# Kernel optimization log

Measured on AMD Instinct MI355X. Metric: run time of the kernel, lower is better.

Reference implementation:

```python
import jax, jax.numpy as jnp
import numpy as np
from jax import lax

B = 8192
NQ = 4  # num_qubits
TWO_PI = 2.0 * np.pi
BN_EPS = 1e-5
ANG_EPS = 1e-6


def setup_inputs() -> dict:
    key = jax.random.key(0)
    ks = jax.random.split(key, 8)
    rn = lambda k, shape, s: jax.random.normal(k, shape, jnp.float32) * s
    return {
        "x": jax.random.normal(ks[0], (B, 1, 28, 28), jnp.float32),
        "conv1_w": rn(ks[1], (8, 1, 3, 3), 0.3),
        "conv1_b": jnp.zeros((8,), jnp.float32),
        "conv2_w": rn(ks[2], (16, 8, 3, 3), 0.1),
        "conv2_b": jnp.zeros((16,), jnp.float32),
        "fc1_w": rn(ks[3], (64, 16 * 7 * 7), 0.04),
        "fc1_b": jnp.zeros((64,), jnp.float32),
        "fc2_w": rn(ks[4], (NQ, 64), 0.12),
        "fc2_b": jnp.zeros((NQ,), jnp.float32),
        "bn_gamma": jnp.ones((NQ,), jnp.float32),
        "bn_beta": jnp.zeros((NQ,), jnp.float32),
        "var_params": jax.random.uniform(ks[5], (3 * NQ,), jnp.float32, 0.0, TWO_PI),
    }


# ---- batched 4-qubit statevector simulation (replaces per-sample Aer loop) ----

def _rx(t):
    c, s = jnp.cos(t / 2), jnp.sin(t / 2)
    return jnp.stack([jnp.stack([c + 0j, -1j * s], -1),
                      jnp.stack([-1j * s, c + 0j], -1)], -2).astype(jnp.complex64)


def _ry(t):
    c, s = jnp.cos(t / 2), jnp.sin(t / 2)
    return jnp.stack([jnp.stack([c, -s], -1),
                      jnp.stack([s, c], -1)], -2).astype(jnp.complex64)


def _rz(t):
    p = jnp.exp(-0.5j * t.astype(jnp.complex64))
    z = jnp.zeros_like(p)
    return jnp.stack([jnp.stack([p, z], -1),
                      jnp.stack([z, jnp.conj(p)], -1)], -2)


def _apply_1q(psi, U, q):
    # psi: [B, 2,2,2,2]; axis q+1 is qubit q. U: [2,2] or [B,2,2].
    psi = jnp.moveaxis(psi, q + 1, 1)
    if U.ndim == 2:
        psi = jnp.einsum('ij,bj...->bi...', U, psi)
    else:
        psi = jnp.einsum('bij,bj...->bi...', U, psi)
    return jnp.moveaxis(psi, 1, q + 1)


def _apply_cnot(psi, c, t):
    ac, at = c + 1, t + 1
    c0 = lax.index_in_dim(psi, 0, ac, keepdims=True)
    c1 = jnp.flip(lax.index_in_dim(psi, 1, ac, keepdims=True), axis=at)
    return jnp.concatenate([c0, c1], axis=ac)


def quantum_expectations(angles, var):
    # angles: [B, NQ] feature angles; var: [3*NQ] shared variational params.
    b = angles.shape[0]
    psi = jnp.zeros((b,) + (2,) * NQ, jnp.complex64)
    psi = psi.at[(slice(None),) + (0,) * NQ].set(1.0)
    for i in range(NQ):                       # Z feature map
        psi = _apply_1q(psi, _rz(angles[:, i]), i)
    for i in range(NQ):                       # RX/RY/RZ ansatz
        psi = _apply_1q(psi, _rx(var[3 * i]), i)
        psi = _apply_1q(psi, _ry(var[3 * i + 1]), i)
        psi = _apply_1q(psi, _rz(var[3 * i + 2]), i)
    for i in range(NQ - 1):                   # linear CNOT chain
        psi = _apply_cnot(psi, i, i + 1)
    p = psi.real ** 2 + psi.imag ** 2          # [B,2,2,2,2] probabilities
    exps = []
    for k in range(NQ):                       # <Z> on qubit k
        axes = tuple(a for a in range(1, NQ + 1) if a != k + 1)
        pk = jnp.sum(p, axis=axes)             # [B,2]
        exps.append(pk[:, 0] - pk[:, 1])
    expZ = jnp.stack(exps, axis=1)             # [B,NQ], qubit-indexed
    # Qiskit Pauli label 'I'*q+'Z'+'I'*(NQ-q-1) puts Z on qubit NQ-1-q -> reverse
    return expZ[:, ::-1]


def _forward(x, conv1_w, conv1_b, conv2_w, conv2_b, fc1_w, fc1_b,
             fc2_w, fc2_b, bn_gamma, bn_beta, var_params):
    dn = ('NCHW', 'OIHW', 'NCHW')
    h = lax.conv_general_dilated(x, conv1_w, (1, 1), 'SAME', dimension_numbers=dn)
    h = jax.nn.relu(h + conv1_b[None, :, None, None])
    h = lax.reduce_window(h, -jnp.inf, lax.max, (1, 1, 2, 2), (1, 1, 2, 2), 'VALID')
    h = lax.conv_general_dilated(h, conv2_w, (1, 1), 'SAME', dimension_numbers=dn)
    h = jax.nn.relu(h + conv2_b[None, :, None, None])
    h = lax.reduce_window(h, -jnp.inf, lax.max, (1, 1, 2, 2), (1, 1, 2, 2), 'VALID')
    feats = h.reshape(h.shape[0], -1)                         # [B, 16*7*7]
    h = jax.nn.relu(feats @ fc1_w.T + fc1_b)
    logits = h @ fc2_w.T + fc2_b                              # [B, NQ]
    # BatchNorm1d (training mode: biased batch stats)
    mu = jnp.mean(logits, axis=0)
    var = jnp.mean((logits - mu) ** 2, axis=0)
    cl = (logits - mu) / jnp.sqrt(var + BN_EPS) * bn_gamma + bn_beta
    # quantum branch is fully detached in the original (numpy round-trip)
    cld = lax.stop_gradient(cl)
    mn = jnp.min(cld, axis=1, keepdims=True)
    mx = jnp.max(cld, axis=1, keepdims=True)
    angles = (cld - mn) / (mx - mn + ANG_EPS) * TWO_PI
    q = lax.stop_gradient(quantum_expectations(angles, var_params))
    return cl + q


def reference(x, conv1_w, conv1_b, conv2_w, conv2_b, fc1_w, fc1_b,
              fc2_w, fc2_b, bn_gamma, bn_beta, var_params):
    return _forward(x, conv1_w, conv1_b, conv2_w, conv2_b, fc1_w, fc1_b,
                    fc2_w, fc2_b, bn_gamma, bn_beta, var_params)
```

## Files before the change

### kernel.cpp

```cpp
#include <hip/hip_runtime.h>
#include <math.h>
#include <stdint.h>

#define BATCH 8192
#define NS 4

typedef _Float16 f16;
typedef _Float16 f16x2 __attribute__((ext_vector_type(2)));
typedef _Float16 f16x8 __attribute__((ext_vector_type(8)));
typedef float f32x4 __attribute__((ext_vector_type(4)));
typedef uint32_t u32x4 __attribute__((ext_vector_type(4)));

__device__ __forceinline__ uint32_t pk2(float a, float b) {
    return __builtin_bit_cast(uint32_t, __builtin_amdgcn_cvt_pkrtz(a, b));
}
__device__ __forceinline__ uint32_t rfl_u(uint32_t v) {
    return (uint32_t)__builtin_amdgcn_readfirstlane((int)v);
}

__global__ __launch_bounds__(256) void fused_cnn(
    const float* __restrict__ x,
    const float* __restrict__ c1w,
    const float* __restrict__ c1b,
    const float* __restrict__ c2w,
    const float* __restrict__ c2b,
    const float* __restrict__ f1w,
    const float* __restrict__ f1b,
    const float* __restrict__ f2w,
    const float* __restrict__ f2b,
    float* __restrict__ logits)
{
    const int tid  = threadIdx.x;
    const int lane = tid & 63;
    const int wid  = tid >> 6;
    const int b0   = blockIdx.x * NS;

    __shared__ __align__(16) f16 h1[NS * 16 * 18 * 8];
    __shared__ __align__(16) f16 sw2a[16 * 96];
    __shared__ __align__(16) unsigned char uni[7680];
    f16*   simg  = (f16*)uni;
    f16*   sfeat = (f16*)uni;
    float* shl   = (float*)(uni + 6400);

    {
        uint32_t* u = (uint32_t*)uni;
        for (int i = tid; i < 1920; i += 256) u[i] = 0;
        uint32_t* h = (uint32_t*)h1;
        for (int i = tid; i < 4608; i += 256) h[i] = 0;
        for (int i = tid; i < 1536; i += 256) {
            int oc = i / 96, kk = i - oc * 96;
            float v = (kk < 72) ? c2w[oc * 72 + (kk & 7) * 9 + (kk >> 3)] : 0.f;
            sw2a[i] = (f16)v;
        }
    }

    f16x2 wpk[36], bpk[4];
#pragma unroll
    for (int t = 0; t < 9; ++t)
#pragma unroll
        for (int pr = 0; pr < 4; ++pr)
            wpk[t * 4 + pr] = __builtin_bit_cast(f16x2,
                rfl_u(pk2(c1w[(2 * pr) * 9 + t], c1w[(2 * pr + 1) * 9 + t])));
#pragma unroll
    for (int pr = 0; pr < 4; ++pr)
        bpk[pr] = __builtin_bit_cast(f16x2, rfl_u(pk2(c1b[2 * pr], c1b[2 * pr + 1])));

    __syncthreads();

#pragma unroll 1
    for (int pass = 0; pass < 4; ++pass) {
        int item = pass * 256 + tid;
        if (item < NS * 196) {
            int s = item / 196, i2 = item - s * 196;
            int r = i2 / 7, c4 = i2 - 7 * r;
            float4 v = *(const float4*)(x + (size_t)(b0 + s) * 784 + r * 28 + c4 * 4);
            f16* dst = simg + (s * 30 + r + 1) * 32 + c4 * 4 + 1;
            dst[0] = (f16)v.x; dst[1] = (f16)v.y; dst[2] = (f16)v.z; dst[3] = (f16)v.w;
        }
    }
    __syncthreads();

#pragma unroll 1
    for (int pass = 0; pass < 4; ++pass) {
        int item = pass * 256 + tid;
        if (item < NS * 196) {
            int s = item / 196, pix = item - s * 196;
            int py = pix / 14, px = pix - 14 * py;
            const f16* ib = simg + (s * 30 + 2 * py) * 32 + 2 * px;
            f16x2 acc[2][2][4];
#pragma unroll
            for (int qy = 0; qy < 2; ++qy)
#pragma unroll
            for (int qx = 0; qx < 2; ++qx)
#pragma unroll
            for (int pr = 0; pr < 4; ++pr) acc[qy][qx][pr] = bpk[pr];

#pragma unroll
            for (int rr = 0; rr < 4; ++rr) {
                f16x2 plo = *(const f16x2*)(ib + rr * 32);
                f16x2 phi = *(const f16x2*)(ib + rr * 32 + 2);
                f16x2 sp[4];
                sp[0][0] = plo[0]; sp[0][1] = plo[0];
                sp[1][0] = plo[1]; sp[1][1] = plo[1];
                sp[2][0] = phi[0]; sp[2][1] = phi[0];
                sp[3][0] = phi[1]; sp[3][1] = phi[1];
#pragma unroll
                for (int qy = 0; qy < 2; ++qy) {
                    int ky = rr - qy;
                    if (ky < 0 || ky > 2) continue;
#pragma unroll
                    for (int qx = 0; qx < 2; ++qx)
#pragma unroll
                    for (int kx = 0; kx < 3; ++kx) {
#pragma unroll
                        for (int pr = 0; pr < 4; ++pr)
                            acc[qy][qx][pr] = __builtin_elementwise_fma(
                                sp[qx + kx], wpk[(ky * 3 + kx) * 4 + pr], acc[qy][qx][pr]);
                    }
                }
            }
            f16x2 z; z[0] = (f16)0.f; z[1] = (f16)0.f;
            uint32_t ov[4];
#pragma unroll
            for (int pr = 0; pr < 4; ++pr) {
                f16x2 m = __builtin_elementwise_max(
                    __builtin_elementwise_max(acc[0][0][pr], acc[0][1][pr]),
                    __builtin_elementwise_max(acc[1][0][pr], acc[1][1][pr]));
                m = __builtin_elementwise_max(m, z);
                ov[pr] = __builtin_bit_cast(uint32_t, m);
            }
            uint4 val = make_uint4(ov[0], ov[1], ov[2], ov[3]);
            *(uint4*)(h1 + ((s * 16 + py + 1) * 18 + (px + 1)) * 8) = val;
        }
    }
    __syncthreads();

    if (tid < 64) sfeat[(tid >> 4) * 800 + 784 + (tid & 15)] = (f16)0.f;

    const int col = lane & 15, grp = lane >> 4;

    {
        const int s = wid;
        const f16* h1b = h1 + s * (16 * 18 * 8);
        const int q = col & 3, pl = col >> 2;
        const int qy = q >> 1, qx = q & 1;
        int koff[3];
#pragma unroll
        for (int st = 0; st < 3; ++st) {
            int t = st * 4 + grp;
            int ky = (t < 9) ? (t / 3) : 0;
            int kx = (t < 9) ? (t - 3 * (t / 3)) : 0;
            koff[st] = (ky * 18 + kx) * 8;
        }
        f16x8 af[3];
#pragma unroll
        for (int st = 0; st < 3; ++st)
            af[st] = *(const f16x8*)(sw2a + col * 96 + st * 32 + grp * 8);
        f32x4 cb;
#pragma unroll
        for (int r = 0; r < 4; ++r) cb[r] = c2b[grp * 4 + r];

#pragma unroll 1
        for (int t = 0; t < 13; ++t) {
            int pc = 4 * t + pl; pc = pc > 48 ? 48 : pc;
            int py = (pc * 9363) >> 16;
            int px = pc - 7 * py;
            const f16* bp = h1b + ((2 * py + qy) * 18 + (2 * px + qx)) * 8;
            f32x4 c = cb;
#pragma unroll
            for (int st = 0; st < 3; ++st) {
                f16x8 bv = *(const f16x8*)(bp + koff[st]);
                c = __builtin_amdgcn_mfma_f32_16x16x32_f16(af[st], bv, c, 0, 0, 0);
            }
            float vr[4];
#pragma unroll
            for (int r = 0; r < 4; ++r) {
                float v = c[r];
                v = fmaxf(v, __shfl_xor(v, 1));
                v = fmaxf(v, __shfl_xor(v, 2));
                vr[r] = fmaxf(v, 0.f);
            }
            int p = 4 * t + pl;
            if (q == 0 && p <= 48) {
#pragma unroll
                for (int r = 0; r < 4; ++r)
                    sfeat[s * 800 + (grp * 4 + r) * 49 + p] = (f16)vr[r];
            }
        }
    }
    __syncthreads();

    {
        const int row = wid * 16 + col;
        const float* wrow = f1w + (size_t)row * 784;
        const int scol = col < NS ? col : 0;
        const f16* fb = sfeat + scol * 800;
        f32x4 c = {0.f, 0.f, 0.f, 0.f};
#pragma unroll 5
        for (int st = 0; st < 25; ++st) {
            int k0 = st * 32 + grp * 8;
            f16x8 a;
            if (k0 < 784) {
                float4 lo = *(const float4*)(wrow + k0);
                float4 hi = *(const float4*)(wrow + k0 + 4);
                u32x4 t = { pk2(lo.x, lo.y), pk2(lo.z, lo.w),
                            pk2(hi.x, hi.y), pk2(hi.z, hi.w) };
                a = __builtin_bit_cast(f16x8, t);
            } else {
                u32x4 t = {0u, 0u, 0u, 0u};
                a = __builtin_bit_cast(f16x8, t);
            }
            f16x8 b = *(const f16x8*)(fb + k0);
            c = __builtin_amdgcn_mfma_f32_16x16x32_f16(a, b, c, 0, 0, 0);
        }
        if (col < NS) {
            float4 h;
            h.x = fmaxf(c[0] + f1b[wid * 16 + grp * 4 + 0], 0.f);
            h.y = fmaxf(c[1] + f1b[wid * 16 + grp * 4 + 1], 0.f);
            h.z = fmaxf(c[2] + f1b[wid * 16 + grp * 4 + 2], 0.f);
            h.w = fmaxf(c[3] + f1b[wid * 16 + grp * 4 + 3], 0.f);
            *(float4*)(shl + col * 64 + wid * 16 + grp * 4) = h;
        }
    }
    __syncthreads();

    {
        const int s = wid;
        float hv = shl[s * 64 + lane];
        float lg[4];
#pragma unroll
        for (int o = 0; o < 4; ++o) {
            float pv = hv * f2w[o * 64 + lane];
#pragma unroll
            for (int sft = 32; sft >= 1; sft >>= 1) pv += __shfl_xor(pv, sft);
            lg[o] = pv + f2b[o];
        }
        if (lane == 0) {
#pragma unroll
            for (int o = 0; o < 4; ++o)
                logits[(size_t)(b0 + s) * 4 + o] = lg[o];
        }
    }
}

__global__ __launch_bounds__(256) void stats_apply(
    const float* __restrict__ logits, const float* __restrict__ var,
    const float* __restrict__ gamma, const float* __restrict__ beta,
    float* __restrict__ out)
{
    const int tid = threadIdx.x;
    const float4* l4 = (const float4*)logits;

    float t[8] = {0, 0, 0, 0, 0, 0, 0, 0};
#pragma unroll 4
    for (int i = 0; i < 32; ++i) {
        float4 v = l4[tid + 256 * i];
        t[0] += v.x; t[1] += v.y; t[2] += v.z; t[3] += v.w;
        t[4] += v.x * v.x; t[5] += v.y * v.y; t[6] += v.z * v.z; t[7] += v.w * v.w;
    }
#pragma unroll
    for (int sft = 32; sft >= 1; sft >>= 1)
#pragma unroll
        for (int j = 0; j < 8; ++j) t[j] += __shfl_xor(t[j], sft);

    __shared__ float part[4][8];
    __shared__ float prm[8];
    if ((tid & 63) == 0) {
#pragma unroll
        for (int j = 0; j < 8; ++j) part[tid >> 6][j] = t[j];
    }
    __syncthreads();

    if (tid == 0) {
        float sums[8];
#pragma unroll
        for (int j = 0; j < 8; ++j)
            sums[j] = part[0][j] + part[1][j] + part[2][j] + part[3][j];

        float pr[16], pi[16];
#pragma unroll
        for (int i = 0; i < 16; ++i) { pr[i] = 0.f; pi[i] = 0.f; }
        pr[0] = 1.f;
        for (int q = 0; q < 4; ++q) {
            float a  = var[3 * q], b_ = var[3 * q + 1], c = var[3 * q + 2];
            float ca = cosf(0.5f * a),  sa = sinf(0.5f * a);
            float cb = cosf(0.5f * b_), sb = sinf(0.5f * b_);
            float cc = cosf(0.5f * c),  sc = sinf(0.5f * c);
            float m00r = cb * ca, m00i =  sb * sa;
            float m01r = -sb * ca, m01i = -cb * sa;
            float m10r =  sb * ca, m10i = -cb * sa;
            float m11r =  cb * ca, m11i = -sb * sa;
            float u00r = cc * m00r + sc * m00i, u00i = cc * m00i - sc * m00r;
            float u01r = cc * m01r + sc * m01i, u01i = cc * m01i - sc * m01r;
            float u10r = cc * m10r - sc * m10i, u10i = cc * m10i + sc * m10r;
            float u11r = cc * m11r - sc * m11i, u11i = cc * m11i + sc * m11r;
            int stq = 1 << (3 - q);
            for (int i = 0; i < 16; ++i) {
                if (i & stq) continue;
                int j = i | stq;
                float xr = pr[i], xi = pi[i], yr = pr[j], yi = pi[j];
                pr[i] = u00r * xr - u00i * xi + u01r * yr - u01i * yi;
                pi[i] = u00r * xi + u00i * xr + u01r * yi + u01i * yr;
                pr[j] = u10r * xr - u10i * xi + u11r * yr - u11i * yi;
                pi[j] = u10r * xi + u10i * xr + u11r * yi + u11i * yr;
            }
        }
        for (int c = 0; c < 3; ++c) {
            int scm = 1 << (3 - c), stm = 1 << (2 - c);
            for (int i = 0; i < 16; ++i) {
                if ((i & scm) && !(i & stm)) {
                    int j = i | stm;
                    float tr = pr[i], ti = pi[i];
                    pr[i] = pr[j]; pi[i] = pi[j];
                    pr[j] = tr;    pi[j] = ti;
                }
            }
        }
        float p[16];
#pragma unroll
        for (int i = 0; i < 16; ++i) p[i] = pr[i] * pr[i] + pi[i] * pi[i];
        float e[4];
        for (int k = 0; k < 4; ++k) {
            float s = 0.f;
            for (int i = 0; i < 16; ++i)
                s += ((i >> (3 - k)) & 1) ? -p[i] : p[i];
            e[k] = s;
        }
        const float invB = 1.0f / (float)BATCH;
        for (int j = 0; j < 4; ++j) {
            float mu   = sums[j] * invB;
            float vr   = sums[4 + j] * invB - mu * mu;
            float istd = 1.0f / sqrtf(vr + 1e-5f);
            float scale = gamma[j] * istd;
            prm[j]     = scale;
            prm[4 + j] = beta[j] - mu * scale + e[3 - j];
        }
    }
    __syncthreads();

    const int smp = blockIdx.x * 256 + tid;
    float4 v = l4[smp];
    float4 r;
    r.x = v.x * prm[0] + prm[4];
    r.y = v.y * prm[1] + prm[5];
    r.z = v.z * prm[2] + prm[6];
    r.w = v.w * prm[3] + prm[7];
    ((float4*)out)[smp] = r;
}

extern "C" void kernel_launch(void* const* d_in, const int* in_sizes, int n_in,
                              void* d_out, int out_size, void* d_ws, size_t ws_size,
                              hipStream_t stream) {
    (void)in_sizes; (void)n_in; (void)out_size; (void)ws_size;
    const float* x   = (const float*)d_in[0];
    const float* c1w = (const float*)d_in[1];
    const float* c1b = (const float*)d_in[2];
    const float* c2w = (const float*)d_in[3];
    const float* c2b = (const float*)d_in[4];
    const float* f1w = (const float*)d_in[5];
    const float* f1b = (const float*)d_in[6];
    const float* f2w = (const float*)d_in[7];
    const float* f2b = (const float*)d_in[8];
    const float* gma = (const float*)d_in[9];
    const float* bta = (const float*)d_in[10];
    const float* var = (const float*)d_in[11];
    float* out = (float*)d_out;

    float* logits = (float*)d_ws;

    fused_cnn<<<BATCH / NS, 256, 0, stream>>>(x, c1w, c1b, c2w, c2b,
                                              f1w, f1b, f2w, f2b, logits);
    stats_apply<<<32, 256, 0, stream>>>(logits, var, gma, bta, out);
}
```

Measured before the change: 149.6 us.

## Process eight samples per block with per-wave private conv pipelines and split-K fc1

Doubles the samples per block to 8 with 512 threads, so each fc1 weight row loaded from global memory is reused across more samples. Each wave now owns one sample through image load, conv1 and conv2, using per-wave LDS regions and lgkmcnt waits in place of block-wide barriers. The conv2 weight fragments are loaded straight from global into registers instead of being staged in LDS. fc1 is split into two K halves across wave pairs, with partial sums reduced through LDS. The cost is a larger LDS footprint and 512-thread blocks, which may lower occupancy, plus an extra barrier and reduction step.

Result: no change. 146.7 us (-1.9%).

```diff
diff --git a/kernel.cpp b/kernel.cpp
--- a/kernel.cpp
+++ b/kernel.cpp
@@ -3,7 +3,7 @@
 #include <stdint.h>
 
 #define BATCH 8192
-#define NS 4
+#define NS 8
 
 typedef _Float16 f16;
 typedef _Float16 f16x2 __attribute__((ext_vector_type(2)));
@@ -17,8 +17,11 @@
 __device__ __forceinline__ uint32_t rfl_u(uint32_t v) {
     return (uint32_t)__builtin_amdgcn_readfirstlane((int)v);
 }
-
-__global__ __launch_bounds__(256) void fused_cnn(
+__device__ __forceinline__ void wave_lds_fence() {
+    asm volatile("s_waitcnt lgkmcnt(0)" ::: "memory");
+}
+
+__global__ __launch_bounds__(512) void fused_cnn(
     const float* __restrict__ x,
     const float* __restrict__ c1w,
     const float* __restrict__ c1b,
@@ -36,22 +39,16 @@
     const int b0   = blockIdx.x * NS;
 
     __shared__ __align__(16) f16 h1[NS * 16 * 18 * 8];
-    __shared__ __align__(16) f16 sw2a[16 * 96];
-    __shared__ __align__(16) unsigned char uni[7680];
-    f16*   simg  = (f16*)uni;
-    f16*   sfeat = (f16*)uni;
-    float* shl   = (float*)(uni + 6400);
-
-    {
-        uint32_t* u = (uint32_t*)uni;
-        for (int i = tid; i < 1920; i += 256) u[i] = 0;
-        uint32_t* h = (uint32_t*)h1;
-        for (int i = tid; i < 4608; i += 256) h[i] = 0;
-        for (int i = tid; i < 1536; i += 256) {
-            int oc = i / 96, kk = i - oc * 96;
-            float v = (kk < 72) ? c2w[oc * 72 + (kk & 7) * 9 + (kk >> 3)] : 0.f;
-            sw2a[i] = (f16)v;
-        }
+    __shared__ __align__(16) unsigned char uni[NS * 1920];
+    float* part = (float*)h1;
+    float* shl  = (float*)((unsigned char*)h1 + 4096);
+
+    {
+        uint4 z = make_uint4(0, 0, 0, 0);
+        uint4* zs = (uint4*)(uni + wid * 1920);
+        for (int i = lane; i < 120; i += 64) zs[i] = z;
+        uint4* zh = (uint4*)(h1 + wid * 2304);
+        for (int i = lane; i < 288; i += 64) zh[i] = z;
     }
 
     f16x2 wpk[36], bpk[4];
@@ -65,83 +62,105 @@
     for (int pr = 0; pr < 4; ++pr)
         bpk[pr] = __builtin_bit_cast(f16x2, rfl_u(pk2(c1b[2 * pr], c1b[2 * pr + 1])));
 
-    __syncthreads();
-
+    const int col = lane & 15, grp = lane >> 4;
+
+    f16x8 af[3];
+#pragma unroll
+    for (int st = 0; st < 3; ++st) {
+        int tap = st * 4 + grp;
+        if (tap < 9) {
+            float tmp[8];
+#pragma unroll
+            for (int j = 0; j < 8; ++j) tmp[j] = c2w[(col * 8 + j) * 9 + tap];
+            u32x4 t = { pk2(tmp[0], tmp[1]), pk2(tmp[2], tmp[3]),
+                        pk2(tmp[4], tmp[5]), pk2(tmp[6], tmp[7]) };
+            af[st] = __builtin_bit_cast(f16x8, t);
+        } else {
+            u32x4 t = {0u, 0u, 0u, 0u};
+            af[st] = __builtin_bit_cast(f16x8, t);
+        }
+    }
+
+    {
+        f16* simg = (f16*)(uni + wid * 1920);
+        const float* xb = x + (size_t)(b0 + wid) * 784;
+        wave_lds_fence();
 #pragma unroll 1
-    for (int pass = 0; pass < 4; ++pass) {
-        int item = pass * 256 + tid;
-        if (item < NS * 196) {
-            int s = item / 196, i2 = item - s * 196;
-            int r = i2 / 7, c4 = i2 - 7 * r;
-            float4 v = *(const float4*)(x + (size_t)(b0 + s) * 784 + r * 28 + c4 * 4);
-            f16* dst = simg + (s * 30 + r + 1) * 32 + c4 * 4 + 1;
-            dst[0] = (f16)v.x; dst[1] = (f16)v.y; dst[2] = (f16)v.z; dst[3] = (f16)v.w;
-        }
-    }
-    __syncthreads();
-
+        for (int pass = 0; pass < 4; ++pass) {
+            int item = pass * 64 + lane;
+            if (item < 196) {
+                int r = item / 7, c4 = item - 7 * r;
+                float4 v = *(const float4*)(xb + r * 28 + c4 * 4);
+                f16* dst = simg + (r + 1) * 32 + c4 * 4 + 1;
+                dst[0] = (f16)v.x; dst[1] = (f16)v.y;
+                dst[2] = (f16)v.z; dst[3] = (f16)v.w;
+            }
+        }
+    }
+    wave_lds_fence();
+
+    {
+        const f16* simg = (const f16*)(uni + wid * 1920);
+        f16* h1s = h1 + wid * 2304;
 #pragma unroll 1
-    for (int pass = 0; pass < 4; ++pass) {
-        int item = pass * 256 + tid;
-        if (item < NS * 196) {
-            int s = item / 196, pix = item - s * 196;
-            int py = pix / 14, px = pix - 14 * py;
-            const f16* ib = simg + (s * 30 + 2 * py) * 32 + 2 * px;
-            f16x2 acc[2][2][4];
-#pragma unroll
-            for (int qy = 0; qy < 2; ++qy)
-#pragma unroll
-            for (int qx = 0; qx < 2; ++qx)
-#pragma unroll
-            for (int pr = 0; pr < 4; ++pr) acc[qy][qx][pr] = bpk[pr];
-
-#pragma unroll
-            for (int rr = 0; rr < 4; ++rr) {
-                f16x2 plo = *(const f16x2*)(ib + rr * 32);
-                f16x2 phi = *(const f16x2*)(ib + rr * 32 + 2);
-                f16x2 sp[4];
-                sp[0][0] = plo[0]; sp[0][1] = plo[0];
-                sp[1][0] = plo[1]; sp[1][1] = plo[1];
-                sp[2][0] = phi[0]; sp[2][1] = phi[0];
-                sp[3][0] = phi[1]; sp[3][1] = phi[1];
-#pragma unroll
-                for (int qy = 0; qy < 2; ++qy) {
-                    int ky = rr - qy;
-                    if (ky < 0 || ky > 2) continue;
-#pragma unroll
-                    for (int qx = 0; qx < 2; ++qx)
-#pragma unroll
-                    for (int kx = 0; kx < 3; ++kx) {
-#pragma unroll
-                        for (int pr = 0; pr < 4; ++pr)
-                            acc[qy][qx][pr] = __builtin_elementwise_fma(
-                                sp[qx + kx], wpk[(ky * 3 + kx) * 4 + pr], acc[qy][qx][pr]);
+        for (int pass = 0; pass < 4; ++pass) {
+            int pix = pass * 64 + lane;
+            if (pix < 196) {
+                int py = pix / 14, px = pix - 14 * py;
+                const f16* ib = simg + (2 * py) * 32 + 2 * px;
+                f16x2 acc[2][2][4];
+#pragma unroll
+                for (int qy = 0; qy < 2; ++qy)
+#pragma unroll
+                for (int qx = 0; qx < 2; ++qx)
+#pragma unroll
+                for (int pr = 0; pr < 4; ++pr) acc[qy][qx][pr] = bpk[pr];
+
+#pragma unroll
+                for (int rr = 0; rr < 4; ++rr) {
+                    f16x2 plo = *(const f16x2*)(ib + rr * 32);
+                    f16x2 phi = *(const f16x2*)(ib + rr * 32 + 2);
+                    f16x2 sp[4];
+                    sp[0][0] = plo[0]; sp[0][1] = plo[0];
+                    sp[1][0] = plo[1]; sp[1][1] = plo[1];
+                    sp[2][0] = phi[0]; sp[2][1] = phi[0];
+                    sp[3][0] = phi[1]; sp[3][1] = phi[1];
+#pragma unroll
+                    for (int qy = 0; qy < 2; ++qy) {
+                        int ky = rr - qy;
+                        if (ky < 0 || ky > 2) continue;
+#pragma unroll
+                        for (int qx = 0; qx < 2; ++qx)
+#pragma unroll
+                        for (int kx = 0; kx < 3; ++kx) {
+#pragma unroll
+                            for (int pr = 0; pr < 4; ++pr)
+                                acc[qy][qx][pr] = __builtin_elementwise_fma(
+                                    sp[qx + kx], wpk[(ky * 3 + kx) * 4 + pr],
+                                    acc[qy][qx][pr]);
+                        }
                     }
                 }
-            }
-            f16x2 z; z[0] = (f16)0.f; z[1] = (f16)0.f;
-            uint32_t ov[4];
-#pragma unroll
-            for (int pr = 0; pr < 4; ++pr) {
-                f16x2 m = __builtin_elementwise_max(
-                    __builtin_elementwise_max(acc[0][0][pr], acc[0][1][pr]),
-                    __builtin_elementwise_max(acc[1][0][pr], acc[1][1][pr]));
-                m = __builtin_elementwise_max(m, z);
-                ov[pr] = __builtin_bit_cast(uint32_t, m);
-            }
-            uint4 val = make_uint4(ov[0], ov[1], ov[2], ov[3]);
-            *(uint4*)(h1 + ((s * 16 + py + 1) * 18 + (px + 1)) * 8) = val;
-        }
-    }
-    __syncthreads();
-
-    if (tid < 64) sfeat[(tid >> 4) * 800 + 784 + (tid & 15)] = (f16)0.f;
-
-    const int col = lane & 15, grp = lane >> 4;
-
-    {
-        const int s = wid;
-        const f16* h1b = h1 + s * (16 * 18 * 8);
+                f16x2 z; z[0] = (f16)0.f; z[1] = (f16)0.f;
+                uint32_t ov[4];
+#pragma unroll
+                for (int pr = 0; pr < 4; ++pr) {
+                    f16x2 m = __builtin_elementwise_max(
+                        __builtin_elementwise_max(acc[0][0][pr], acc[0][1][pr]),
+                        __builtin_elementwise_max(acc[1][0][pr], acc[1][1][pr]));
+                    m = __builtin_elementwise_max(m, z);
+                    ov[pr] = __builtin_bit_cast(uint32_t, m);
+                }
+                uint4 val = make_uint4(ov[0], ov[1], ov[2], ov[3]);
+                *(uint4*)(h1s + ((py + 1) * 18 + (px + 1)) * 8) = val;
+            }
+        }
+    }
+    wave_lds_fence();
+
+    {
+        const f16* h1b = h1 + wid * 2304;
+        f16* sfeats = (f16*)uni + wid * 968;
         const int q = col & 3, pl = col >> 2;
         const int qy = q >> 1, qx = q & 1;
         int koff[3];
@@ -152,10 +171,6 @@
             int kx = (t < 9) ? (t - 3 * (t / 3)) : 0;
             koff[st] = (ky * 18 + kx) * 8;
         }
-        f16x8 af[3];
-#pragma unroll
-        for (int st = 0; st < 3; ++st)
-            af[st] = *(const f16x8*)(sw2a + col * 96 + st * 32 + grp * 8);
         f32x4 cb;
 #pragma unroll
         for (int r = 0; r < 4; ++r) cb[r] = c2b[grp * 4 + r];
@@ -184,21 +199,25 @@
             if (q == 0 && p <= 48) {
 #pragma unroll
                 for (int r = 0; r < 4; ++r)
-                    sfeat[s * 800 + (grp * 4 + r) * 49 + p] = (f16)vr[r];
-            }
-        }
-    }
-    __syncthreads();
-
-    {
-        const int row = wid * 16 + col;
+                    sfeats[(grp * 4 + r) * 49 + p] = (f16)vr[r];
+            }
+        }
+        if (lane < 8) *(uint32_t*)(sfeats + 784 + lane * 2) = 0u;
+    }
+    __syncthreads();
+
+    {
+        const int rt = wid & 3, kh = wid >> 2;
+        const int row = rt * 16 + col;
         const float* wrow = f1w + (size_t)row * 784;
+        const int kbase = kh * 416;
+        const int steps = 13 - kh;
         const int scol = col < NS ? col : 0;
-        const f16* fb = sfeat + scol * 800;
+        const f16* fb = (const f16*)uni + scol * 968;
         f32x4 c = {0.f, 0.f, 0.f, 0.f};
-#pragma unroll 5
-        for (int st = 0; st < 25; ++st) {
-            int k0 = st * 32 + grp * 8;
+#pragma unroll 4
+        for (int st = 0; st < steps; ++st) {
+            int k0 = kbase + st * 32 + grp * 8;
             f16x8 a;
             if (k0 < 784) {
                 float4 lo = *(const float4*)(wrow + k0);
@@ -214,19 +233,22 @@
             c = __builtin_amdgcn_mfma_f32_16x16x32_f16(a, b, c, 0, 0, 0);
         }
         if (col < NS) {
-            float4 h;
-            h.x = fmaxf(c[0] + f1b[wid * 16 + grp * 4 + 0], 0.f);
-            h.y = fmaxf(c[1] + f1b[wid * 16 + grp * 4 + 1], 0.f);
-            h.z = fmaxf(c[2] + f1b[wid * 16 + grp * 4 + 2], 0.f);
-            h.w = fmaxf(c[3] + f1b[wid * 16 + grp * 4 + 3], 0.f);
-            *(float4*)(shl + col * 64 + wid * 16 + grp * 4) = h;
-        }
-    }
-    __syncthreads();
-
-    {
-        const int s = wid;
-        float hv = shl[s * 64 + lane];
+#pragma unroll
+            for (int r = 0; r < 4; ++r)
+                part[kh * 512 + (rt * 16 + grp * 4 + r) * 8 + col] = c[r];
+        }
+    }
+    __syncthreads();
+
+    {
+        const int m = tid >> 3, sm = tid & 7;
+        float v = part[m * 8 + sm] + part[512 + m * 8 + sm] + f1b[m];
+        shl[sm * 64 + m] = fmaxf(v, 0.f);
+    }
+    __syncthreads();
+
+    {
+        float hv = shl[wid * 64 + lane];
         float lg[4];
 #pragma unroll
         for (int o = 0; o < 4; ++o) {
@@ -236,9 +258,8 @@
             lg[o] = pv + f2b[o];
         }
         if (lane == 0) {
-#pragma unroll
-            for (int o = 0; o < 4; ++o)
-                logits[(size_t)(b0 + s) * 4 + o] = lg[o];
+            float4 out4 = make_float4(lg[0], lg[1], lg[2], lg[3]);
+            *(float4*)(logits + (size_t)(b0 + wid) * 4) = out4;
         }
     }
 }
@@ -368,7 +389,7 @@
 
     float* logits = (float*)d_ws;
 
-    fused_cnn<<<BATCH / NS, 256, 0, stream>>>(x, c1w, c1b, c2w, c2b,
+    fused_cnn<<<BATCH / NS, 512, 0, stream>>>(x, c1w, c1b, c2w, c2b,
                                               f1w, f1b, f2w, f2b, logits);
     stats_apply<<<32, 256, 0, stream>>>(logits, var, gma, bta, out);
 }
```
